# Performance work log

Hardware: AMD Instinct MI355X
Metric: run time of the kernel (lower is better)

The kernel has to match this reference:

```python
import jax, jax.numpy as jnp
import numpy as np

MARGIN = 1.0
MAX_TRIALS = 50


def setup_inputs() -> dict:
    key = jax.random.key(0)
    k1, k2 = jax.random.split(key)
    B = 1048576
    scores = jax.random.normal(k1, (B,), dtype=jnp.float32)
    labels = jax.random.randint(k2, (B,), 0, 2, dtype=jnp.int64)
    return {"scores": scores, "labels": labels}


def reference(scores, labels):
    # Vectorized WARP: the sequential rejection-sampling loop draws i.i.d.
    # uniform negatives until a margin violation; equivalently we pre-draw
    # max_trials negatives per example and take the first violating one.
    B = scores.shape[0]
    lab = labels.astype(jnp.int32)
    num_pos = jnp.sum(lab == 1)
    num_neg = jnp.sum(lab == 0)

    # stable argsort puts label-0 (negative) positions first
    order = jnp.argsort(lab)

    key = jax.random.key(42)
    u = jax.random.uniform(key, (B, MAX_TRIALS), dtype=jnp.float32)
    # uniform index into the negative pool (num_neg is traced -> use floor(u*n))
    idx = jnp.minimum((u * num_neg.astype(jnp.float32)).astype(jnp.int32),
                      jnp.maximum(num_neg - 1, 0))
    neg_idx = order[idx]                       # (B, T) positions of sampled negatives
    neg_samples = scores[neg_idx]              # (B, T)

    violates = neg_samples + MARGIN > scores[:, None]   # (B, T)
    any_viol = jnp.any(violates, axis=1)
    trials = jnp.argmax(violates, axis=1)      # number of failed trials before hit
    neg_at = jnp.take_along_axis(neg_samples, trials[:, None], axis=1)[:, 0]

    # rank_est = max(1, max_trials // (trials + 1)); weight = H(rank_est)
    rank_est = jnp.maximum(1, MAX_TRIALS // (trials + 1))
    harmonics = jnp.cumsum(1.0 / jnp.arange(1, MAX_TRIALS + 1, dtype=scores.dtype))
    weight = harmonics[rank_est - 1]

    per = weight * jnp.maximum(MARGIN - (scores - neg_at), 0.0)
    per = jnp.where((lab == 1) & any_viol, per, 0.0)
    total = jnp.sum(per)

    valid = (num_pos > 0) & (num_neg > 0)
    return jnp.where(valid, total / jnp.maximum(num_pos, 1).astype(scores.dtype), 0.0)
```

## Files before the change

kernel.cpp:

```cpp
#include <hip/hip_runtime.h>
#include <stdint.h>

#define MAX_TRIALS 50
#define MARGIN 1.0f

#define SBLOCK 256
#define SEG 1024
#define MBLOCK 1024
#define MME 2
#define MCHUNK (MBLOCK * MME)

#define FLAG_AGG 1ULL
#define FLAG_INC 2ULL

__device__ __forceinline__ uint32_t rotl32(uint32_t x, uint32_t d) {
  return (x << d) | (x >> (32u - d));
}

__device__ __forceinline__ uint32_t threefry_0_42(uint32_t x0, uint32_t x1, int which) {
  const uint32_t k0 = 0u, k1 = 42u;
  const uint32_t k2 = k0 ^ k1 ^ 0x1BD11BDAu;
  const uint32_t ks[3] = {k0, k1, k2};
  const uint32_t rotA[4] = {13u, 15u, 26u, 6u};
  const uint32_t rotB[4] = {17u, 29u, 16u, 24u};
  x0 += ks[0];
  x1 += ks[1];
#pragma unroll
  for (int r = 0; r < 5; ++r) {
#pragma unroll
    for (int j = 0; j < 4; ++j) {
      uint32_t rot = (r & 1) ? rotB[j] : rotA[j];
      x0 += x1;
      x1 = rotl32(x1, rot);
      x1 ^= x0;
    }
    x0 += ks[(r + 1) % 3];
    x1 += ks[(r + 2) % 3] + (uint32_t)(r + 1);
  }
  return which ? x1 : x0;
}

__device__ __forceinline__ float sample_u(uint32_t j, uint32_t half) {
  uint32_t x0, x1;
  int which;
  if (j < half) { x0 = j; x1 = j + half; which = 0; }
  else          { x0 = j - half; x1 = j; which = 1; }
  uint32_t bits = threefry_0_42(x0, x1, which);
  return __uint_as_float((bits >> 9) | 0x3f800000u) - 1.0f;
}

__global__ void __launch_bounds__(SBLOCK) scan_scatter_kernel(
    const float* __restrict__ scores, const int* __restrict__ labels,
    unsigned long long* __restrict__ desc, int* __restrict__ counters,
    float* __restrict__ negScores, float* __restrict__ out, int B, int nseg) {
  __shared__ int s_scan[SBLOCK];
  __shared__ int s_base;
  const int t = threadIdx.x;
  const int seg = blockIdx.x;

  if (seg == 0 && t == 0) out[0] = 0.0f;

  int e0 = seg * SEG + 4 * t;
  int lab[4] = {1, 1, 1, 1};
  float sc[4] = {0.f, 0.f, 0.f, 0.f};
  if (e0 + 3 < B) {
    int4 L = *reinterpret_cast<const int4*>(labels + e0);
    float4 S = *reinterpret_cast<const float4*>(scores + e0);
    lab[0] = L.x; lab[1] = L.y; lab[2] = L.z; lab[3] = L.w;
    sc[0] = S.x; sc[1] = S.y; sc[2] = S.z; sc[3] = S.w;
  } else {
    for (int k = 0; k < 4; ++k) {
      int e = e0 + k;
      if (e < B) { lab[k] = labels[e]; sc[k] = scores[e]; }
    }
  }
  int c = (lab[0] == 0) + (lab[1] == 0) + (lab[2] == 0) + (lab[3] == 0);
  s_scan[t] = c;
  __syncthreads();
  for (int d = 1; d < SBLOCK; d <<= 1) {
    int v = (t >= d) ? s_scan[t - d] : 0;
    __syncthreads();
    s_scan[t] += v;
    __syncthreads();
  }
  const int cnt = s_scan[SBLOCK - 1];

  if (seg == 0) {
    if (t == 0) {
      atomicExch(&desc[0], (FLAG_INC << 32) | (unsigned)cnt);
      s_base = 0;
      if (nseg == 1) counters[0] = cnt;
    }
  } else {
    if (t == 0) atomicExch(&desc[seg], (FLAG_AGG << 32) | (unsigned)cnt);
    if (t < 64) {
      int running = 0;
      int w = 0;
      bool done = false;
      while (!done) {
        int idx = seg - 1 - w * 64 - t;
        unsigned flag;
        int val;
        do {
          if (idx >= 0) {
            unsigned long long v = atomicAdd(&desc[idx], 0ULL);
            flag = (unsigned)(v >> 32);
            val = (int)(unsigned)v;
          } else {
            flag = (unsigned)FLAG_INC;
            val = 0;
          }
        } while (!__all(flag == 1u || flag == 2u));
        unsigned long long incmask = __ballot(flag == 2u);
        int contrib;
        if (incmask) {
          int l = __ffsll(incmask) - 1;
          contrib = (t <= l) ? val : 0;
          done = true;
        } else {
          contrib = val;
          ++w;
        }
#pragma unroll
        for (int off = 32; off > 0; off >>= 1) contrib += __shfl_down(contrib, off, 64);
        if (t == 0) running += contrib;
      }
      if (t == 0) {
        atomicExch(&desc[seg], (FLAG_INC << 32) | (unsigned)(running + cnt));
        s_base = running;
        if (seg == nseg - 1) counters[0] = running + cnt;
      }
    }
  }
  __syncthreads();
  const int base = s_base;

  int pos = base + s_scan[t] - c;
  for (int k = 0; k < 4; ++k)
    if (lab[k] == 0) negScores[pos++] = sc[k];
}

__global__ void __launch_bounds__(MBLOCK, 8) warp_main(
    const float* __restrict__ scores, const int* __restrict__ labels,
    const float* __restrict__ negScores, const int* __restrict__ counters,
    float* __restrict__ out, int B) {
  __shared__ float H[MAX_TRIALS + 1];
  __shared__ int s_qe[MCHUNK];
  __shared__ float s_qs[MCHUNK];
  __shared__ int s_ci[MCHUNK];
  __shared__ int s_qn;
  __shared__ int s_cn;
  __shared__ float s_bsum[MBLOCK / 64];

  const int tid = threadIdx.x;
  const int lane = tid & 63;
  const int wave = tid >> 6;
  const int nwaves = MBLOCK / 64;

  if (tid == 0) {
    float a = 0.0f;
    for (int k = 1; k <= MAX_TRIALS; ++k) { a += 1.0f / (float)k; H[k] = a; }
    s_qn = 0;
    s_cn = 0;
  }
  __syncthreads();

  const int num_neg = counters[0];
  if (num_neg == 0) return;

  const float fneg = (float)num_neg;
  const uint32_t half = (uint32_t)(((unsigned long long)B * MAX_TRIALS) >> 1);

  float acc = 0.0f;
  int my_e[MME];
  float my_s[MME];
  int nsurv = 0;

  int e0 = blockIdx.x * MCHUNK + 2 * tid;
  int lab[2] = {1, 1};
  float sc[2] = {0.f, 0.f};
  if (e0 + 1 < B) {
    int2 L = *reinterpret_cast<const int2*>(labels + e0);
    float2 S = *reinterpret_cast<const float2*>(scores + e0);
    lab[0] = L.x; lab[1] = L.y;
    sc[0] = S.x; sc[1] = S.y;
  } else {
    for (int k = 0; k < 2; ++k) {
      int e = e0 + k;
      if (e < B) { lab[k] = labels[e]; sc[k] = scores[e]; }
    }
  }
  float n0[2], n1[2];
#pragma unroll
  for (int k = 0; k < 2; ++k) {
    if (lab[k] == 1) {
      uint32_t jb = (uint32_t)(e0 + k) * (uint32_t)MAX_TRIALS;
      float u0 = sample_u(jb, half);
      float u1 = sample_u(jb + 1u, half);
      int g0 = (int)(u0 * fneg);
      int g1 = (int)(u1 * fneg);
      if (g0 > num_neg - 1) g0 = num_neg - 1;
      if (g1 > num_neg - 1) g1 = num_neg - 1;
      n0[k] = negScores[g0];
      n1[k] = negScores[g1];
    }
  }
#pragma unroll
  for (int k = 0; k < 2; ++k) {
    if (lab[k] == 1) {
      float s = sc[k];
      if (n0[k] + MARGIN > s) {
        float h = MARGIN - (s - n0[k]);
        if (h < 0.0f) h = 0.0f;
        acc += H[50] * h;
      } else if (n1[k] + MARGIN > s) {
        float h = MARGIN - (s - n1[k]);
        if (h < 0.0f) h = 0.0f;
        acc += H[25] * h;
      } else {
        my_e[nsurv] = e0 + k;
        my_s[nsurv] = s;
        ++nsurv;
      }
    }
  }

  int qp = 0;
  if (nsurv) qp = atomicAdd(&s_qn, nsurv);
  for (int i = 0; i < nsurv; ++i) {
    s_qe[qp + i] = my_e[i];
    s_qs[qp + i] = my_s[i];
  }
  __syncthreads();

  const int qn = s_qn;
  for (int q = wave * 2; q < qn; q += nwaves * 2) {
    int which = lane >> 5;
    int qi = q + which;
    bool have = (qi < qn);
    float sq = 0.0f;
    int eq = 0;
    if (have) { sq = s_qs[qi]; eq = s_qe[qi]; }
    int t = 2 + (lane & 31);
    bool viol = false;
    float neg = 0.0f;
    if (have) {
      float u = sample_u((uint32_t)eq * (uint32_t)MAX_TRIALS + (uint32_t)t, half);
      int idx = (int)(u * fneg);
      if (idx > num_neg - 1) idx = num_neg - 1;
      neg = negScores[idx];
      viol = (neg + MARGIN > sq);
    }
    unsigned long long vm = __ballot(viol);
    unsigned myhalf = (unsigned)(vm >> (which * 32));
    if (have) {
      if (myhalf) {
        int f = __ffs(myhalf) - 1;
        if ((lane & 31) == f) {
          int trials = 2 + f;
          int rank = MAX_TRIALS / (trials + 1);
          float h = MARGIN - (sq - neg);
          if (h < 0.0f) h = 0.0f;
          acc += H[rank] * h;
        }
      } else if ((lane & 31) == 0) {
        s_ci[atomicAdd(&s_cn, 1)] = qi;
      }
    }
  }
  __syncthreads();

  const int cn = s_cn;
  for (int c = wave; c < cn; c += nwaves) {
    int qi = s_ci[c];
    float sq = s_qs[qi];
    int eq = s_qe[qi];
    bool viol = false;
    float neg = 0.0f;
    if (lane < 16) {
      int t = 34 + lane;
      float u = sample_u((uint32_t)eq * (uint32_t)MAX_TRIALS + (uint32_t)t, half);
      int idx = (int)(u * fneg);
      if (idx > num_neg - 1) idx = num_neg - 1;
      neg = negScores[idx];
      viol = (neg + MARGIN > sq);
    }
    unsigned long long vm = __ballot(viol);
    if (vm) {
      int f = __ffsll(vm) - 1;
      if (lane == f) {
        float h = MARGIN - (sq - neg);
        if (h < 0.0f) h = 0.0f;
        acc += H[1] * h;
      }
    }
  }

  float v = acc;
#pragma unroll
  for (int off = 32; off > 0; off >>= 1) v += __shfl_down(v, off, 64);
  if (lane == 0) s_bsum[wave] = v;
  __syncthreads();
  if (tid == 0) {
    int np = B - num_neg;
    if (np > 0) {
      float bs = 0.0f;
      for (int i = 0; i < MBLOCK / 64; ++i) bs += s_bsum[i];
      atomicAdd(out, bs * (1.0f / (float)np));
    }
  }
}

extern "C" void kernel_launch(void* const* d_in, const int* in_sizes, int n_in,
                              void* d_out, int out_size, void* d_ws, size_t ws_size,
                              hipStream_t stream) {
  const float* scores = (const float*)d_in[0];
  const int* labels = (const int*)d_in[1];
  int B = in_sizes[0];
  int nseg = (B + SEG - 1) / SEG;
  int nb2 = (B + MCHUNK - 1) / MCHUNK;

  char* ws = (char*)d_ws;
  int* counters = (int*)ws;
  unsigned long long* desc = (unsigned long long*)(ws + 64);
  float* negScores = (float*)(ws + 64 + 8 * 1024);

  scan_scatter_kernel<<<nseg, SBLOCK, 0, stream>>>(scores, labels, desc, counters,
                                                   negScores, (float*)d_out, B, nseg);
  warp_main<<<nb2, MBLOCK, 0, stream>>>(scores, labels, negScores, counters,
                                        (float*)d_out, B);
}
```

Before: 86.79 us.

## Pair elements e and e+B/2 to share threefry outputs; use shuffle-based block scan

JAX's threefry produces both output words from one hash of the counter pair (j, j+half). For element e, trial t uses counter e*50+t; for element e+B/2 it is e*50+t+half. A thread can therefore handle elements e and e+B/2 and get both of their first two uniforms from two hash calls instead of four. This is used when B is even, with the old layout kept as a fallback for odd B. Separately, the scatter kernel's LDS Hillis-Steele scan is replaced by a wavefront shuffle scan plus per-wave sums, which removes many block barriers. The cost is less contiguous, non-vectorised loads of labels and scores.

```diff
diff --git a/kernel.cpp b/kernel.cpp
--- a/kernel.cpp
+++ b/kernel.cpp
@@ -7,8 +7,7 @@
 #define SBLOCK 256
 #define SEG 1024
 #define MBLOCK 1024
-#define MME 2
-#define MCHUNK (MBLOCK * MME)
+#define MCHUNK (MBLOCK * 2)
 
 #define FLAG_AGG 1ULL
 #define FLAG_INC 2ULL
@@ -17,7 +16,8 @@
   return (x << d) | (x >> (32u - d));
 }
 
-__device__ __forceinline__ uint32_t threefry_0_42(uint32_t x0, uint32_t x1, int which) {
+__device__ __forceinline__ void threefry2_0_42(uint32_t x0, uint32_t x1,
+                                               uint32_t* o0, uint32_t* o1) {
   const uint32_t k0 = 0u, k1 = 42u;
   const uint32_t k2 = k0 ^ k1 ^ 0x1BD11BDAu;
   const uint32_t ks[3] = {k0, k1, k2};
@@ -37,25 +37,32 @@
     x0 += ks[(r + 1) % 3];
     x1 += ks[(r + 2) % 3] + (uint32_t)(r + 1);
   }
-  return which ? x1 : x0;
+  *o0 = x0;
+  *o1 = x1;
+}
+
+__device__ __forceinline__ float bits_to_u(uint32_t bits) {
+  return __uint_as_float((bits >> 9) | 0x3f800000u) - 1.0f;
 }
 
 __device__ __forceinline__ float sample_u(uint32_t j, uint32_t half) {
-  uint32_t x0, x1;
+  uint32_t x0, x1, o0, o1;
   int which;
   if (j < half) { x0 = j; x1 = j + half; which = 0; }
   else          { x0 = j - half; x1 = j; which = 1; }
-  uint32_t bits = threefry_0_42(x0, x1, which);
-  return __uint_as_float((bits >> 9) | 0x3f800000u) - 1.0f;
+  threefry2_0_42(x0, x1, &o0, &o1);
+  return bits_to_u(which ? o1 : o0);
 }
 
 __global__ void __launch_bounds__(SBLOCK) scan_scatter_kernel(
     const float* __restrict__ scores, const int* __restrict__ labels,
     unsigned long long* __restrict__ desc, int* __restrict__ counters,
     float* __restrict__ negScores, float* __restrict__ out, int B, int nseg) {
-  __shared__ int s_scan[SBLOCK];
+  __shared__ int s_wsum[4];
   __shared__ int s_base;
   const int t = threadIdx.x;
+  const int lane = t & 63;
+  const int wave = t >> 6;
   const int seg = blockIdx.x;
 
   if (seg == 0 && t == 0) out[0] = 0.0f;
@@ -74,16 +81,20 @@
       if (e < B) { lab[k] = labels[e]; sc[k] = scores[e]; }
     }
   }
-  int c = (lab[0] == 0) + (lab[1] == 0) + (lab[2] == 0) + (lab[3] == 0);
-  s_scan[t] = c;
-  __syncthreads();
-  for (int d = 1; d < SBLOCK; d <<= 1) {
-    int v = (t >= d) ? s_scan[t - d] : 0;
-    __syncthreads();
-    s_scan[t] += v;
-    __syncthreads();
-  }
-  const int cnt = s_scan[SBLOCK - 1];
+  const int c = (lab[0] == 0) + (lab[1] == 0) + (lab[2] == 0) + (lab[3] == 0);
+
+  int incl = c;
+#pragma unroll
+  for (int d = 1; d < 64; d <<= 1) {
+    int o = __shfl_up(incl, d, 64);
+    if (lane >= d) incl += o;
+  }
+  if (lane == 63) s_wsum[wave] = incl;
+  __syncthreads();
+  const int cnt = s_wsum[0] + s_wsum[1] + s_wsum[2] + s_wsum[3];
+  int woff = 0;
+  for (int w = 0; w < wave; ++w) woff += s_wsum[w];
+  incl += woff;
 
   if (seg == 0) {
     if (t == 0) {
@@ -135,12 +146,12 @@
   __syncthreads();
   const int base = s_base;
 
-  int pos = base + s_scan[t] - c;
+  int pos = base + incl - c;
   for (int k = 0; k < 4; ++k)
     if (lab[k] == 0) negScores[pos++] = sc[k];
 }
 
-__global__ void __launch_bounds__(MBLOCK, 8) warp_main(
+__global__ void __launch_bounds__(MBLOCK, 8) warp_main_paired(
     const float* __restrict__ scores, const int* __restrict__ labels,
     const float* __restrict__ negScores, const int* __restrict__ counters,
     float* __restrict__ out, int B) {
@@ -170,57 +181,56 @@
 
   const float fneg = (float)num_neg;
   const uint32_t half = (uint32_t)(((unsigned long long)B * MAX_TRIALS) >> 1);
+  const int Hh = B >> 1;
 
   float acc = 0.0f;
-  int my_e[MME];
-  float my_s[MME];
+  int my_e[2];
+  float my_s[2];
   int nsurv = 0;
 
-  int e0 = blockIdx.x * MCHUNK + 2 * tid;
-  int lab[2] = {1, 1};
-  float sc[2] = {0.f, 0.f};
-  if (e0 + 1 < B) {
-    int2 L = *reinterpret_cast<const int2*>(labels + e0);
-    float2 S = *reinterpret_cast<const float2*>(scores + e0);
-    lab[0] = L.x; lab[1] = L.y;
-    sc[0] = S.x; sc[1] = S.y;
-  } else {
+  const int elo = blockIdx.x * MBLOCK + tid;
+  if (elo < Hh) {
+    const int ehi = elo + Hh;
+    int lb[2];
+    float ss[2];
+    lb[0] = labels[elo]; lb[1] = labels[ehi];
+    ss[0] = scores[elo]; ss[1] = scores[ehi];
+    const uint32_t jb = (uint32_t)elo * (uint32_t)MAX_TRIALS;
+    uint32_t a0, b0, a1, b1;
+    threefry2_0_42(jb, jb + half, &a0, &b0);
+    threefry2_0_42(jb + 1u, jb + 1u + half, &a1, &b1);
+    float u0[2] = {bits_to_u(a0), bits_to_u(b0)};
+    float u1[2] = {bits_to_u(a1), bits_to_u(b1)};
+    const int ee[2] = {elo, ehi};
+    float n0[2], n1[2];
+#pragma unroll
     for (int k = 0; k < 2; ++k) {
-      int e = e0 + k;
-      if (e < B) { lab[k] = labels[e]; sc[k] = scores[e]; }
-    }
-  }
-  float n0[2], n1[2];
-#pragma unroll
-  for (int k = 0; k < 2; ++k) {
-    if (lab[k] == 1) {
-      uint32_t jb = (uint32_t)(e0 + k) * (uint32_t)MAX_TRIALS;
-      float u0 = sample_u(jb, half);
-      float u1 = sample_u(jb + 1u, half);
-      int g0 = (int)(u0 * fneg);
-      int g1 = (int)(u1 * fneg);
-      if (g0 > num_neg - 1) g0 = num_neg - 1;
-      if (g1 > num_neg - 1) g1 = num_neg - 1;
-      n0[k] = negScores[g0];
-      n1[k] = negScores[g1];
-    }
-  }
-#pragma unroll
-  for (int k = 0; k < 2; ++k) {
-    if (lab[k] == 1) {
-      float s = sc[k];
-      if (n0[k] + MARGIN > s) {
-        float h = MARGIN - (s - n0[k]);
-        if (h < 0.0f) h = 0.0f;
-        acc += H[50] * h;
-      } else if (n1[k] + MARGIN > s) {
-        float h = MARGIN - (s - n1[k]);
-        if (h < 0.0f) h = 0.0f;
-        acc += H[25] * h;
-      } else {
-        my_e[nsurv] = e0 + k;
-        my_s[nsurv] = s;
-        ++nsurv;
+      if (lb[k] == 1) {
+        int g0 = (int)(u0[k] * fneg);
+        int g1 = (int)(u1[k] * fneg);
+        if (g0 > num_neg - 1) g0 = num_neg - 1;
+        if (g1 > num_neg - 1) g1 = num_neg - 1;
+        n0[k] = negScores[g0];
+        n1[k] = negScores[g1];
+      }
+    }
+#pragma unroll
+    for (int k = 0; k < 2; ++k) {
+      if (lb[k] == 1) {
+        float s = ss[k];
+        if (n0[k] + MARGIN > s) {
+          float h = MARGIN - (s - n0[k]);
+          if (h < 0.0f) h = 0.0f;
+          acc += H[50] * h;
+        } else if (n1[k] + MARGIN > s) {
+          float h = MARGIN - (s - n1[k]);
+          if (h < 0.0f) h = 0.0f;
+          acc += H[25] * h;
+        } else {
+          my_e[nsurv] = ee[k];
+          my_s[nsurv] = s;
+          ++nsurv;
+        }
       }
     }
   }
@@ -311,6 +321,177 @@
   }
 }
 
+__global__ void __launch_bounds__(MBLOCK, 8) warp_main_generic(
+    const float* __restrict__ scores, const int* __restrict__ labels,
+    const float* __restrict__ negScores, const int* __restrict__ counters,
+    float* __restrict__ out, int B) {
+  __shared__ float H[MAX_TRIALS + 1];
+  __shared__ int s_qe[MCHUNK];
+  __shared__ float s_qs[MCHUNK];
+  __shared__ int s_ci[MCHUNK];
+  __shared__ int s_qn;
+  __shared__ int s_cn;
+  __shared__ float s_bsum[MBLOCK / 64];
+
+  const int tid = threadIdx.x;
+  const int lane = tid & 63;
+  const int wave = tid >> 6;
+  const int nwaves = MBLOCK / 64;
+
+  if (tid == 0) {
+    float a = 0.0f;
+    for (int k = 1; k <= MAX_TRIALS; ++k) { a += 1.0f / (float)k; H[k] = a; }
+    s_qn = 0;
+    s_cn = 0;
+  }
+  __syncthreads();
+
+  const int num_neg = counters[0];
+  if (num_neg == 0) return;
+
+  const float fneg = (float)num_neg;
+  const uint32_t half = (uint32_t)(((unsigned long long)B * MAX_TRIALS) >> 1);
+
+  float acc = 0.0f;
+  int my_e[2];
+  float my_s[2];
+  int nsurv = 0;
+
+  int e0 = blockIdx.x * MCHUNK + 2 * tid;
+  int lab[2] = {1, 1};
+  float sc[2] = {0.f, 0.f};
+  if (e0 + 1 < B) {
+    int2 L = *reinterpret_cast<const int2*>(labels + e0);
+    float2 S = *reinterpret_cast<const float2*>(scores + e0);
+    lab[0] = L.x; lab[1] = L.y;
+    sc[0] = S.x; sc[1] = S.y;
+  } else {
+    for (int k = 0; k < 2; ++k) {
+      int e = e0 + k;
+      if (e < B) { lab[k] = labels[e]; sc[k] = scores[e]; }
+    }
+  }
+  float n0[2], n1[2];
+#pragma unroll
+  for (int k = 0; k < 2; ++k) {
+    if (lab[k] == 1) {
+      uint32_t jb = (uint32_t)(e0 + k) * (uint32_t)MAX_TRIALS;
+      float u0 = sample_u(jb, half);
+      float u1 = sample_u(jb + 1u, half);
+      int g0 = (int)(u0 * fneg);
+      int g1 = (int)(u1 * fneg);
+      if (g0 > num_neg - 1) g0 = num_neg - 1;
+      if (g1 > num_neg - 1) g1 = num_neg - 1;
+      n0[k] = negScores[g0];
+      n1[k] = negScores[g1];
+    }
+  }
+#pragma unroll
+  for (int k = 0; k < 2; ++k) {
+    if (lab[k] == 1) {
+      float s = sc[k];
+      if (n0[k] + MARGIN > s) {
+        float h = MARGIN - (s - n0[k]);
+        if (h < 0.0f) h = 0.0f;
+        acc += H[50] * h;
+      } else if (n1[k] + MARGIN > s) {
+        float h = MARGIN - (s - n1[k]);
+        if (h < 0.0f) h = 0.0f;
+        acc += H[25] * h;
+      } else {
+        my_e[nsurv] = e0 + k;
+        my_s[nsurv] = s;
+        ++nsurv;
+      }
+    }
+  }
+
+  int qp = 0;
+  if (nsurv) qp = atomicAdd(&s_qn, nsurv);
+  for (int i = 0; i < nsurv; ++i) {
+    s_qe[qp + i] = my_e[i];
+    s_qs[qp + i] = my_s[i];
+  }
+  __syncthreads();
+
+  const int qn = s_qn;
+  for (int q = wave * 2; q < qn; q += nwaves * 2) {
+    int which = lane >> 5;
+    int qi = q + which;
+    bool have = (qi < qn);
+    float sq = 0.0f;
+    int eq = 0;
+    if (have) { sq = s_qs[qi]; eq = s_qe[qi]; }
+    int t = 2 + (lane & 31);
+    bool viol = false;
+    float neg = 0.0f;
+    if (have) {
+      float u = sample_u((uint32_t)eq * (uint32_t)MAX_TRIALS + (uint32_t)t, half);
+      int idx = (int)(u * fneg);
+      if (idx > num_neg - 1) idx = num_neg - 1;
+      neg = negScores[idx];
+      viol = (neg + MARGIN > sq);
+    }
+    unsigned long long vm = __ballot(viol);
+    unsigned myhalf = (unsigned)(vm >> (which * 32));
+    if (have) {
+      if (myhalf) {
+        int f = __ffs(myhalf) - 1;
+        if ((lane & 31) == f) {
+          int trials = 2 + f;
+          int rank = MAX_TRIALS / (trials + 1);
+          float h = MARGIN - (sq - neg);
+          if (h < 0.0f) h = 0.0f;
+          acc += H[rank] * h;
+        }
+      } else if ((lane & 31) == 0) {
+        s_ci[atomicAdd(&s_cn, 1)] = qi;
+      }
+    }
+  }
+  __syncthreads();
+
+  const int cn = s_cn;
+  for (int c = wave; c < cn; c += nwaves) {
+    int qi = s_ci[c];
+    float sq = s_qs[qi];
+    int eq = s_qe[qi];
+    bool viol = false;
+    float neg = 0.0f;
+    if (lane < 16) {
+      int t = 34 + lane;
+      float u = sample_u((uint32_t)eq * (uint32_t)MAX_TRIALS + (uint32_t)t, half);
+      int idx = (int)(u * fneg);
+      if (idx > num_neg - 1) idx = num_neg - 1;
+      neg = negScores[idx];
+      viol = (neg + MARGIN > sq);
+    }
+    unsigned long long vm = __ballot(viol);
+    if (vm) {
+      int f = __ffsll(vm) - 1;
+      if (lane == f) {
+        float h = MARGIN - (sq - neg);
+        if (h < 0.0f) h = 0.0f;
+        acc += H[1] * h;
+      }
+    }
+  }
+
+  float v = acc;
+#pragma unroll
+  for (int off = 32; off > 0; off >>= 1) v += __shfl_down(v, off, 64);
+  if (lane == 0) s_bsum[wave] = v;
+  __syncthreads();
+  if (tid == 0) {
+    int np = B - num_neg;
+    if (np > 0) {
+      float bs = 0.0f;
+      for (int i = 0; i < MBLOCK / 64; ++i) bs += s_bsum[i];
+      atomicAdd(out, bs * (1.0f / (float)np));
+    }
+  }
+}
+
 extern "C" void kernel_launch(void* const* d_in, const int* in_sizes, int n_in,
                               void* d_out, int out_size, void* d_ws, size_t ws_size,
                               hipStream_t stream) {
@@ -318,7 +499,6 @@
   const int* labels = (const int*)d_in[1];
   int B = in_sizes[0];
   int nseg = (B + SEG - 1) / SEG;
-  int nb2 = (B + MCHUNK - 1) / MCHUNK;
 
   char* ws = (char*)d_ws;
   int* counters = (int*)ws;
@@ -327,6 +507,13 @@
 
   scan_scatter_kernel<<<nseg, SBLOCK, 0, stream>>>(scores, labels, desc, counters,
                                                    negScores, (float*)d_out, B, nseg);
-  warp_main<<<nb2, MBLOCK, 0, stream>>>(scores, labels, negScores, counters,
-                                        (float*)d_out, B);
-}
+  if ((B & 1) == 0) {
+    int nbp = ((B >> 1) + MBLOCK - 1) / MBLOCK;
+    warp_main_paired<<<nbp, MBLOCK, 0, stream>>>(scores, labels, negScores, counters,
+                                                 (float*)d_out, B);
+  } else {
+    int nbg = (B + MCHUNK - 1) / MCHUNK;
+    warp_main_generic<<<nbg, MBLOCK, 0, stream>>>(scores, labels, negScores, counters,
+                                                  (float*)d_out, B);
+  }
+}
```

New measurement: 85.88 us. No clear change (-1.0%).
